# Performance work log

Hardware: AMD Instinct MI355X
Metric: run time of the kernel (lower is better)

## Reference

```python
import jax, jax.numpy as jnp
import numpy as np

NEG_SLOPE = 0.2  # PyG GATConv default negative_slope


def gat_conv(x, src, dst, W, a_src, a_dst, b, n_nodes, concat):
    # x: [N, F_in]; W: [F_in, H*C]; a_src/a_dst: [H, C]; b: [H*C] or [C]
    H, C = a_src.shape
    h = (x @ W).reshape(n_nodes, H, C)                      # [N, H, C]
    al_src = jnp.sum(h * a_src[None], axis=-1)              # [N, H]
    al_dst = jnp.sum(h * a_dst[None], axis=-1)              # [N, H]
    e = jax.nn.leaky_relu(al_src[src] + al_dst[dst], NEG_SLOPE)  # [E, H]
    # segment softmax over incoming edges of each destination node
    m = jax.ops.segment_max(e, dst, num_segments=n_nodes)  # [N, H]
    ex = jnp.exp(e - m[dst])                                # [E, H]
    s = jax.ops.segment_sum(ex, dst, num_segments=n_nodes)  # [N, H]
    alpha = ex / s[dst]                                     # [E, H]
    msg = h[src] * alpha[:, :, None]                        # [E, H, C]
    out = jax.ops.segment_sum(msg, dst, num_segments=n_nodes)  # [N, H, C]
    if concat:
        out = out.reshape(n_nodes, H * C)
    else:
        out = out.mean(axis=1)
    return out + b


def setup_inputs() -> dict:
    key = jax.random.key(0)
    ks = jax.random.split(key, 10)
    N, E = 100000, 800000
    F_in, C1, H, C2 = 128, 32, 8, 16
    x = jax.random.normal(ks[0], (N, F_in), dtype=jnp.float32)
    edge_index = jax.random.randint(ks[1], (2, E), 0, N, dtype=jnp.int64)
    s = 0.05
    return {
        "x": x,
        "edge_index": edge_index,
        "W1": jax.random.normal(ks[2], (F_in, H * C1), dtype=jnp.float32) * s,
        "att_src1": jax.random.normal(ks[3], (H, C1), dtype=jnp.float32) * s,
        "att_dst1": jax.random.normal(ks[4], (H, C1), dtype=jnp.float32) * s,
        "b1": jnp.zeros((H * C1,), dtype=jnp.float32),
        "W2": jax.random.normal(ks[5], (H * C1, H * C2), dtype=jnp.float32) * s,
        "att_src2": jax.random.normal(ks[6], (H, C2), dtype=jnp.float32) * s,
        "att_dst2": jax.random.normal(ks[7], (H, C2), dtype=jnp.float32) * s,
        "b2": jnp.zeros((C2,), dtype=jnp.float32),
    }


def reference(x, edge_index, W1, att_src1, att_dst1, b1, W2, att_src2, att_dst2, b2):
    n = x.shape[0]
    # PyG GATConv default add_self_loops=True (same augmented edge set for both layers)
    loops = jnp.arange(n, dtype=edge_index.dtype)
    src = jnp.concatenate([edge_index[0], loops])
    dst = jnp.concatenate([edge_index[1], loops])
    # dropout_p = 0.0 -> dropout is identity (eval-mode math)
    h = gat_conv(x, src, dst, W1, att_src1, att_dst1, b1, n, concat=True)
    h = jax.nn.elu(h)
    out = gat_conv(h, src, dst, W2, att_src2, att_dst2, b2, n, concat=False)
    return jax.nn.log_softmax(out, axis=-1)
```

## Files before the change

### kernel.cpp

```cpp
#include <hip/hip_runtime.h>
#include <cstdint>
#include <cstddef>


typedef short bf16x8 __attribute__((ext_vector_type(8)));
typedef unsigned short u16x8 __attribute__((ext_vector_type(8)));
typedef float f32x4 __attribute__((ext_vector_type(4)));

__device__ inline unsigned short f2bf(float f) {
  unsigned u = __float_as_uint(f);
  unsigned r = (u + 0x7FFFu + ((u >> 16) & 1u)) >> 16;
  return (unsigned short)r;
}
__device__ inline float bf2f(unsigned short s) {
  return __uint_as_float((unsigned)s << 16);
}

__device__ inline unsigned char fp8enc(float x) {
  unsigned u = __float_as_uint(x);
  unsigned s = u >> 31;
  float ax = fminf(fabsf(x), 448.f);
  unsigned em;
  if (ax >= 0.015625f) {
    unsigned b = __float_as_uint(ax);
    unsigned b2 = b + 0x7FFFFu + ((b >> 20) & 1u);
    em = (b2 >> 20) - 960u;
    if (em > 126u) em = 126u;
  } else {
    em = (unsigned)__float2int_rn(ax * 512.f);
  }
  return (unsigned char)((s << 7) | em);
}
__device__ inline float fp8dec_sw(unsigned b8) {
  unsigned s = b8 >> 7, em = b8 & 0x7Fu;
  float fn = __uint_as_float((s << 31) | ((em + 960u) << 20));
  float fd = (float)em * 0.001953125f;
  fd = s ? -fd : fd;
  return em >= 8u ? fn : fd;
}
__device__ inline void fp8dec4(unsigned w, float* out) {
#if __has_builtin(__builtin_amdgcn_cvt_f32_fp8)
  out[0] = __builtin_amdgcn_cvt_f32_fp8(w, 0);
  out[1] = __builtin_amdgcn_cvt_f32_fp8(w, 1);
  out[2] = __builtin_amdgcn_cvt_f32_fp8(w, 2);
  out[3] = __builtin_amdgcn_cvt_f32_fp8(w, 3);
#else
  out[0] = fp8dec_sw(w & 0xFFu);
  out[1] = fp8dec_sw((w >> 8) & 0xFFu);
  out[2] = fp8dec_sw((w >> 16) & 0xFFu);
  out[3] = fp8dec_sw((w >> 24) & 0xFFu);
#endif
}


__global__ __launch_bounds__(256) void detect_kernel(const int* __restrict__ words,
                                                     int E, int* __restrict__ flag) {
  int t = threadIdx.x;
  int n = E < 1024 ? E : 1024;
  int cnt = 0;
  for (int i = t; i < n; i += 256) cnt += (words[2 * i + 1] != 0) ? 1 : 0;
  for (int m = 1; m < 64; m <<= 1) cnt += __shfl_xor(cnt, m);
  if ((t & 63) == 0 && cnt) atomicAdd(flag, cnt);
}

__global__ __launch_bounds__(256) void scan_a(const int* __restrict__ deg,
                                              int* __restrict__ off,
                                              int* __restrict__ bsum, int N) {
  __shared__ int sh[256];
  int b = blockIdx.x, t = threadIdx.x;
  int base = b * 2048 + t * 8;
  int p[8];
  int run = 0;
#pragma unroll
  for (int j = 0; j < 8; ++j) {
    int v = (base + j < N) ? deg[base + j] : 0;
    run += v;
    p[j] = run;
  }
  sh[t] = run;
  __syncthreads();
  for (int d = 1; d < 256; d <<= 1) {
    int x = (t >= d) ? sh[t - d] : 0;
    __syncthreads();
    if (t >= d) sh[t] += x;
    __syncthreads();
  }
  int excl = sh[t] - run;
#pragma unroll
  for (int j = 0; j < 8; ++j)
    if (base + j < N) off[base + j + 1] = excl + p[j];
  if (t == 255) bsum[b] = sh[255];
}

__global__ __launch_bounds__(256) void scan_c(int* __restrict__ off,
                                              const int* __restrict__ bsum,
                                              int N, int nb) {
  __shared__ int sb[64];
  int t = threadIdx.x;
  if (t < 64) {
    int v = (t < nb) ? bsum[t] : 0;
    for (int d = 1; d < 64; d <<= 1) {
      int u = __shfl_up(v, d);
      if (t >= d) v += u;
    }
    sb[t] = v;
  }
  __syncthreads();
  int i = blockIdx.x * 256 + t;
  if (i == 0) off[0] = 0;
  if (i >= 1 && i <= N) {
    int c = (i - 1) / 2048;
    int excl = (c == 0) ? 0 : sb[c - 1];
    off[i] += excl;
  }
}

__global__ __launch_bounds__(256) void fill_kernel(const int* __restrict__ src,
                                                   const int* __restrict__ dst,
                                                   const int* __restrict__ off,
                                                   int* __restrict__ deg,
                                                   int* __restrict__ csr, int ET) {
  int e = blockIdx.x * 256 + threadIdx.x;
  if (e >= ET) return;
  int d = dst[e];
  int p = atomicSub(&deg[d], 1) - 1;
  csr[off[d] + p] = src[e];
}

__device__ inline void pack_one(const float* __restrict__ W,
                                short* __restrict__ Wp, int NOUT, int idx) {
  int NT = NOUT >> 4;
  int j = idx & 7;
  int lane = (idx >> 3) & 63;
  int st = idx >> 9;
  int s = st / NT, t = st - s * NT;
  int k = s * 32 + (lane >> 4) * 8 + j;
  int n = t * 16 + (lane & 15);
  Wp[idx] = (short)f2bf(W[(size_t)k * NOUT + n]);
}

__global__ __launch_bounds__(256) void pack2_kernel(const float* __restrict__ W1,
                                                    short* __restrict__ W1p,
                                                    const float* __restrict__ W2,
                                                    short* __restrict__ W2p) {
  int b = blockIdx.x, t = threadIdx.x;
  if (b < 128) pack_one(W1, W1p, 256, b * 256 + t);
  else         pack_one(W2, W2p, 128, (b - 128) * 256 + t);
}

template <int K, int NOUT, bool AF32>
__device__ void gemm_body(int bx, const void* __restrict__ Av,
                          const short* __restrict__ Bp,
                          unsigned char* __restrict__ Cq,
                          const float* __restrict__ as,
                          const float* __restrict__ ad,
                          float* __restrict__ alsO,
                          float* __restrict__ aldO, int M) {
  constexpr int KS = K / 32;
  constexpr int NT = NOUT / 16;
  constexpr int RST = NOUT + 8;
  constexpr int QST = NOUT + 16;
  constexpr int C = NOUT / 8;
  __shared__ __align__(16) short lds[64 * RST];
  __shared__ __align__(16) unsigned char ldsq[64 * QST];
  const int tid = threadIdx.x;
  const int wave = tid >> 6, lane = tid & 63;
  const int lo = lane & 15, hi = lane >> 4;
  const int rowA = bx * 64 + wave * 16 + lo;
  const bool inb = rowA < M;

  f32x4 acc[NT];
#pragma unroll
  for (int t = 0; t < NT; ++t) acc[t] = (f32x4){0.f, 0.f, 0.f, 0.f};

#pragma unroll
  for (int s = 0; s < KS; ++s) {
    bf16x8 af;
    if constexpr (AF32) {
      const float* Ap = (const float*)Av;
      float v[8];
      if (inb) {
        const float4 x0 = *(const float4*)&Ap[(size_t)rowA * K + s * 32 + hi * 8];
        const float4 x1 = *(const float4*)&Ap[(size_t)rowA * K + s * 32 + hi * 8 + 4];
        v[0] = x0.x; v[1] = x0.y; v[2] = x0.z; v[3] = x0.w;
        v[4] = x1.x; v[5] = x1.y; v[6] = x1.z; v[7] = x1.w;
      } else {
#pragma unroll
        for (int j = 0; j < 8; ++j) v[j] = 0.f;
      }
#pragma unroll
      for (int j = 0; j < 8; ++j) af[j] = (short)f2bf(v[j]);
    } else {
      const short* Ab = (const short*)Av;
      if (inb) {
        af = *(const bf16x8*)&Ab[(size_t)rowA * K + s * 32 + hi * 8];
      } else {
#pragma unroll
        for (int j = 0; j < 8; ++j) af[j] = 0;
      }
    }
#pragma unroll
    for (int t = 0; t < NT; ++t) {
      bf16x8 bf = *(const bf16x8*)&Bp[((size_t)(s * NT + t) * 64 + lane) * 8];
      acc[t] = __builtin_amdgcn_mfma_f32_16x16x32_bf16(af, bf, acc[t], 0, 0, 0);
    }
  }

#pragma unroll
  for (int t = 0; t < NT; ++t)
#pragma unroll
    for (int r = 0; r < 4; ++r) {
      int row = wave * 16 + hi * 4 + r;
      lds[row * RST + t * 16 + lo] = (short)f2bf(acc[t][r]);
      ldsq[row * QST + t * 16 + lo] = fp8enc(acc[t][r]);
    }
  __syncthreads();

  constexpr int CPR = NOUT / 16;
#pragma unroll
  for (int i = 0; i < (64 * CPR) / 256; ++i) {
    int v = i * 256 + tid;
    int r = v / CPR;
    int c = v % CPR;
    int grow = bx * 64 + r;
    if (grow < M)
      *(float4*)&Cq[(size_t)grow * NOUT + c * 16] =
          *(const float4*)&ldsq[r * QST + c * 16];
  }

  constexpr int SEGS = NOUT / 64;
  if (tid < 64 * SEGS) {
    int r = tid / SEGS, seg = tid % SEGS;
    int grow = bx * 64 + r;
    float ps[8], pd[8];
#pragma unroll
    for (int k = 0; k < 8; ++k) { ps[k] = 0.f; pd[k] = 0.f; }
#pragma unroll
    for (int k = 0; k < 8; ++k) {
      int b = seg + SEGS * k;
      u16x8 u = *(const u16x8*)&lds[r * RST + b * 8];
#pragma unroll
      for (int j = 0; j < 8; ++j) {
        float hv = bf2f(u[j]);
        ps[k] = fmaf(hv, as[k * C + seg * 8 + j], ps[k]);
        pd[k] = fmaf(hv, ad[k * C + seg * 8 + j], pd[k]);
      }
    }
#pragma unroll
    for (int d = 1; d < SEGS; d <<= 1)
#pragma unroll
      for (int k = 0; k < 8; ++k) {
        ps[k] += __shfl_xor(ps[k], d);
        pd[k] += __shfl_xor(pd[k], d);
      }
    if (seg == 0 && grow < M) {
      *(float4*)&alsO[(size_t)grow * 8] = make_float4(ps[0], ps[1], ps[2], ps[3]);
      *(float4*)&alsO[(size_t)grow * 8 + 4] = make_float4(ps[4], ps[5], ps[6], ps[7]);
      *(float4*)&aldO[(size_t)grow * 8] = make_float4(pd[0], pd[1], pd[2], pd[3]);
      *(float4*)&aldO[(size_t)grow * 8 + 4] = make_float4(pd[4], pd[5], pd[6], pd[7]);
    }
  }
}

__global__ __launch_bounds__(256) void mega1_kernel(
    const float* __restrict__ x, const short* __restrict__ W1p,
    unsigned char* __restrict__ h1q, const float* __restrict__ as1,
    const float* __restrict__ ad1, float* __restrict__ als,
    float* __restrict__ ald, int M, int gemmGrid,
    const void* __restrict__ ei, int E, int N, const int* __restrict__ flag,
    int* __restrict__ src, int* __restrict__ dst, int* __restrict__ deg) {
  int bx = blockIdx.x;
  if (bx < gemmGrid) {
    gemm_body<128, 256, true>(bx, x, W1p, h1q, as1, ad1, als, ald, M);
  } else {
    int e = (bx - gemmGrid) * 256 + threadIdx.x;
    int ET = E + N;
    if (e >= ET) return;
    int s, d;
    if (e < E) {
      if (flag[0] == 0) {
        const long long* p = (const long long*)ei;
        s = (int)p[e];
        d = (int)p[(size_t)E + e];
      } else {
        const int* p = (const int*)ei;
        s = p[e];
        d = p[E + e];
      }
    } else {
      s = d = e - E;
    }
    src[e] = s;
    dst[e] = d;
    atomicAdd(&deg[d], 1);
  }
}

template <int K, int NOUT, bool AF32>
__global__ __launch_bounds__(256) void mfma_gemm(const void* __restrict__ Av,
                                                 const short* __restrict__ Bp,
                                                 unsigned char* __restrict__ Cq,
                                                 const float* __restrict__ as,
                                                 const float* __restrict__ ad,
                                                 float* __restrict__ alsO,
                                                 float* __restrict__ aldO, int M) {
  gemm_body<K, NOUT, AF32>(blockIdx.x, Av, Bp, Cq, as, ad, alsO, aldO, M);
}

__global__ __launch_bounds__(256) void agg1_kernel(const unsigned char* __restrict__ hq,
                                                   const float* __restrict__ als,
                                                   const float* __restrict__ ald,
                                                   const int* __restrict__ off,
                                                   const int* __restrict__ csr,
                                                   const float* __restrict__ bias,
                                                   short* __restrict__ outb, int N) {
  int wid = blockIdx.x * 4 + (threadIdx.x >> 6);
  if (wid >= N) return;
  int lane = threadIdx.x & 63;
  int rs = off[wid], re = off[wid + 1];
  int es = lane >> 5;
  int gl = lane & 31;
  int head = gl >> 2;
  float aldv = ald[wid * 8 + head];

  float acc[8];
#pragma unroll
  for (int j = 0; j < 8; ++j) acc[j] = 0.f;
  float ws = 0.f;

  int i = rs + es;
  for (; i + 2 < re; i += 4) {
    int s0 = csr[i], s1 = csr[i + 2];
    float e0 = als[s0 * 8 + head] + aldv;
    float e1 = als[s1 * 8 + head] + aldv;
    uint2 u0 = *(const uint2*)&hq[(size_t)s0 * 256 + gl * 8];
    uint2 u1 = *(const uint2*)&hq[(size_t)s1 * 256 + gl * 8];
    e0 = fmaxf(e0, 0.2f * e0);
    e1 = fmaxf(e1, 0.2f * e1);
    float w0 = __expf(e0), w1 = __expf(e1);
    ws += w0 + w1;
    float d0a[4], d0b[4], d1a[4], d1b[4];
    fp8dec4(u0.x, d0a); fp8dec4(u0.y, d0b);
    fp8dec4(u1.x, d1a); fp8dec4(u1.y, d1b);
#pragma unroll
    for (int j = 0; j < 4; ++j) {
      acc[j] = fmaf(w0, d0a[j], acc[j]);
      acc[j + 4] = fmaf(w0, d0b[j], acc[j + 4]);
      acc[j] = fmaf(w1, d1a[j], acc[j]);
      acc[j + 4] = fmaf(w1, d1b[j], acc[j + 4]);
    }
  }
  if (i < re) {
    int s0 = csr[i];
    float e0 = als[s0 * 8 + head] + aldv;
    uint2 u0 = *(const uint2*)&hq[(size_t)s0 * 256 + gl * 8];
    e0 = fmaxf(e0, 0.2f * e0);
    float w0 = __expf(e0);
    ws += w0;
    float d0a[4], d0b[4];
    fp8dec4(u0.x, d0a); fp8dec4(u0.y, d0b);
#pragma unroll
    for (int j = 0; j < 4; ++j) {
      acc[j] = fmaf(w0, d0a[j], acc[j]);
      acc[j + 4] = fmaf(w0, d0b[j], acc[j + 4]);
    }
  }

  ws += __shfl_xor(ws, 32);
#pragma unroll
  for (int j = 0; j < 8; ++j) acc[j] += __shfl_xor(acc[j], 32);
  float inv = 1.f / ws;

  if (lane < 32) {
    u16x8 o;
#pragma unroll
    for (int j = 0; j < 8; ++j) {
      float v = acc[j] * inv + bias[gl * 8 + j];
      o[j] = f2bf(v > 0.f ? v : expm1f(v));
    }
    *(u16x8*)&outb[(size_t)wid * 256 + gl * 8] = o;
  }
}

__global__ __launch_bounds__(256) void agg2_kernel(const unsigned char* __restrict__ hq,
                                                   const float* __restrict__ als,
                                                   const float* __restrict__ ald,
                                                   const int* __restrict__ off,
                                                   const int* __restrict__ csr,
                                                   const float* __restrict__ bias,
                                                   float* __restrict__ out, int N) {
  int wid = blockIdx.x * 4 + (threadIdx.x >> 6);
  if (wid >= N) return;
  int lane = threadIdx.x & 63;
  int rs = off[wid], re = off[wid + 1];
  int es = lane >> 4;
  int gl = lane & 15;
  int head = gl >> 1;
  float aldv = ald[wid * 8 + head];

  float acc[8];
#pragma unroll
  for (int j = 0; j < 8; ++j) acc[j] = 0.f;
  float ws = 0.f;

  int i = rs + es;
  for (; i + 4 < re; i += 8) {
    int s0 = csr[i], s1 = csr[i + 4];
    float e0 = als[s0 * 8 + head] + aldv;
    float e1 = als[s1 * 8 + head] + aldv;
    uint2 u0 = *(const uint2*)&hq[(size_t)s0 * 128 + gl * 8];
    uint2 u1 = *(const uint2*)&hq[(size_t)s1 * 128 + gl * 8];
    e0 = fmaxf(e0, 0.2f * e0);
    e1 = fmaxf(e1, 0.2f * e1);
    float w0 = __expf(e0), w1 = __expf(e1);
    ws += w0 + w1;
    float d0[8], d1[8];
    fp8dec4(u0.x, d0); fp8dec4(u0.y, d0 + 4);
    fp8dec4(u1.x, d1); fp8dec4(u1.y, d1 + 4);
#pragma unroll
    for (int j = 0; j < 8; ++j)
      acc[j] = fmaf(w1, d1[j], fmaf(w0, d0[j], acc[j]));
  }
  if (i < re) {
    int s0 = csr[i];
    float e0 = als[s0 * 8 + head] + aldv;
    uint2 u0 = *(const uint2*)&hq[(size_t)s0 * 128 + gl * 8];
    e0 = fmaxf(e0, 0.2f * e0);
    float w0 = __expf(e0);
    ws += w0;
    float d0[8];
    fp8dec4(u0.x, d0); fp8dec4(u0.y, d0 + 4);
#pragma unroll
    for (int j = 0; j < 8; ++j) acc[j] = fmaf(w0, d0[j], acc[j]);
  }

#pragma unroll
  for (int d = 16; d < 64; d <<= 1) {
    ws += __shfl_xor(ws, d);
#pragma unroll
    for (int j = 0; j < 8; ++j) acc[j] += __shfl_xor(acc[j], d);
  }
  float inv = 1.f / ws;

#pragma unroll
  for (int j = 0; j < 8; ++j) acc[j] *= inv;
#pragma unroll
  for (int d = 2; d <= 8; d <<= 1)
#pragma unroll
    for (int j = 0; j < 8; ++j) acc[j] += __shfl_xor(acc[j], d);
  int p = gl & 1;
  float v[8];
#pragma unroll
  for (int j = 0; j < 8; ++j) v[j] = acc[j] * 0.125f + bias[p * 8 + j];
  float m = v[0];
#pragma unroll
  for (int j = 1; j < 8; ++j) m = fmaxf(m, v[j]);
  m = fmaxf(m, __shfl_xor(m, 1));
  float se = 0.f;
#pragma unroll
  for (int j = 0; j < 8; ++j) se += __expf(v[j] - m);
  se += __shfl_xor(se, 1);
  float lse = m + logf(se);
  if (lane < 2) {
    *(float4*)&out[(size_t)wid * 16 + p * 8] =
        make_float4(v[0] - lse, v[1] - lse, v[2] - lse, v[3] - lse);
    *(float4*)&out[(size_t)wid * 16 + p * 8 + 4] =
        make_float4(v[4] - lse, v[5] - lse, v[6] - lse, v[7] - lse);
  }
}


extern "C" void kernel_launch(void* const* d_in, const int* in_sizes, int n_in,
                              void* d_out, int out_size, void* d_ws, size_t ws_size,
                              hipStream_t stream) {
  const float* x = (const float*)d_in[0];
  const void* ei = d_in[1];
  const float* W1 = (const float*)d_in[2];
  const float* as1 = (const float*)d_in[3];
  const float* ad1 = (const float*)d_in[4];
  const float* b1 = (const float*)d_in[5];
  const float* W2 = (const float*)d_in[6];
  const float* as2 = (const float*)d_in[7];
  const float* ad2 = (const float*)d_in[8];
  const float* b2 = (const float*)d_in[9];
  float* out = (float*)d_out;

  const int N = out_size / 16;
  const int E = in_sizes[1] / 2;
  const int ET = E + N;

  char* p = (char*)d_ws;
  auto alloc = [&](size_t bytes) {
    char* r = p;
    p += (bytes + 255) & ~(size_t)255;
    return (void*)r;
  };
  unsigned char* h1q = (unsigned char*)alloc((size_t)N * 256);
  short* hactb = (short*)alloc((size_t)N * 256 * 2);
  float* als = (float*)alloc((size_t)N * 8 * 4);
  float* ald = (float*)alloc((size_t)N * 8 * 4);
  int* src32 = (int*)alloc((size_t)ET * 4);
  int* dst32 = (int*)alloc((size_t)ET * 4);
  int* csr = (int*)alloc((size_t)ET * 4);
  int* deg = (int*)alloc((size_t)N * 4);
  int* flag = (int*)alloc(256);
  int* off = (int*)alloc((size_t)(N + 1) * 4);
  int* bsum = (int*)alloc(256 * 4);
  short* W1p = (short*)alloc(128 * 256 * 2);
  short* W2p = (short*)alloc(256 * 128 * 2);
  unsigned char* h2q = h1q;

  hipMemsetAsync(deg, 0, (((size_t)N * 4 + 255) & ~(size_t)255) + 4, stream);

  detect_kernel<<<1, 256, 0, stream>>>((const int*)ei, E, flag);
  pack2_kernel<<<256, 256, 0, stream>>>(W1, W1p, W2, W2p);

  int gemmGrid = (N + 63) / 64;
  int gridET = (ET + 255) / 256;
  int nodeGrid = (N + 3) / 4;
  int nscan = (N + 2047) / 2048;

  mega1_kernel<<<gemmGrid + gridET, 256, 0, stream>>>(
      x, W1p, h1q, as1, ad1, als, ald, N, gemmGrid, ei, E, N, flag, src32,
      dst32, deg);
  scan_a<<<nscan, 256, 0, stream>>>(deg, off, bsum, N);
  scan_c<<<(N + 256) / 256, 256, 0, stream>>>(off, bsum, N, nscan);
  fill_kernel<<<gridET, 256, 0, stream>>>(src32, dst32, off, deg, csr, ET);

  agg1_kernel<<<nodeGrid, 256, 0, stream>>>(h1q, als, ald, off, csr, b1, hactb, N);
  mfma_gemm<256, 128, false><<<gemmGrid, 256, 0, stream>>>(
      hactb, W2p, h2q, as2, ad2, als, ald, N);
  agg2_kernel<<<nodeGrid, 256, 0, stream>>>(h2q, als, ald, off, csr, b2, out, N);
}
```

Before: 324.6 us.

## Split layer-1 aggregation across channel halves and fold detect into pack kernel

```diff
diff --git a/kernel.cpp b/kernel.cpp
--- a/kernel.cpp
+++ b/kernel.cpp
@@ -53,16 +53,6 @@
 }
 
 
-__global__ __launch_bounds__(256) void detect_kernel(const int* __restrict__ words,
-                                                     int E, int* __restrict__ flag) {
-  int t = threadIdx.x;
-  int n = E < 1024 ? E : 1024;
-  int cnt = 0;
-  for (int i = t; i < n; i += 256) cnt += (words[2 * i + 1] != 0) ? 1 : 0;
-  for (int m = 1; m < 64; m <<= 1) cnt += __shfl_xor(cnt, m);
-  if ((t & 63) == 0 && cnt) atomicAdd(flag, cnt);
-}
-
 __global__ __launch_bounds__(256) void scan_a(const int* __restrict__ deg,
                                               int* __restrict__ off,
                                               int* __restrict__ bsum, int N) {
@@ -142,10 +132,21 @@
 __global__ __launch_bounds__(256) void pack2_kernel(const float* __restrict__ W1,
                                                     short* __restrict__ W1p,
                                                     const float* __restrict__ W2,
-                                                    short* __restrict__ W2p) {
+                                                    short* __restrict__ W2p,
+                                                    const int* __restrict__ words,
+                                                    int E, int* __restrict__ flag) {
   int b = blockIdx.x, t = threadIdx.x;
-  if (b < 128) pack_one(W1, W1p, 256, b * 256 + t);
-  else         pack_one(W2, W2p, 128, (b - 128) * 256 + t);
+  if (b < 128) {
+    pack_one(W1, W1p, 256, b * 256 + t);
+  } else if (b < 256) {
+    pack_one(W2, W2p, 128, (b - 128) * 256 + t);
+  } else {
+    int n = E < 1024 ? E : 1024;
+    int cnt = 0;
+    for (int i = t; i < n; i += 256) cnt += (words[2 * i + 1] != 0) ? 1 : 0;
+    for (int m = 1; m < 64; m <<= 1) cnt += __shfl_xor(cnt, m);
+    if ((t & 63) == 0 && cnt) atomicAdd(flag, cnt);
+  }
 }
 
 template <int K, int NOUT, bool AF32>
@@ -316,11 +317,13 @@
                                                    short* __restrict__ outb, int N) {
   int wid = blockIdx.x * 4 + (threadIdx.x >> 6);
   if (wid >= N) return;
+  int cb = blockIdx.y;
   int lane = threadIdx.x & 63;
   int rs = off[wid], re = off[wid + 1];
-  int es = lane >> 5;
-  int gl = lane & 31;
-  int head = gl >> 2;
+  int es = lane >> 4;
+  int gl = lane & 15;
+  int chb = cb * 128 + gl * 8;
+  int head = chb >> 5;
   float aldv = ald[wid * 8 + head];
 
   float acc[8];
@@ -329,56 +332,53 @@
   float ws = 0.f;
 
   int i = rs + es;
-  for (; i + 2 < re; i += 4) {
-    int s0 = csr[i], s1 = csr[i + 2];
-    float e0 = als[s0 * 8 + head] + aldv;
-    float e1 = als[s1 * 8 + head] + aldv;
-    uint2 u0 = *(const uint2*)&hq[(size_t)s0 * 256 + gl * 8];
-    uint2 u1 = *(const uint2*)&hq[(size_t)s1 * 256 + gl * 8];
+  for (; i + 4 < re; i += 8) {
+    int s0 = csr[i], s1 = csr[i + 4];
+    float a0 = als[s0 * 8 + head];
+    float a1 = als[s1 * 8 + head];
+    uint2 u0 = *(const uint2*)&hq[(size_t)s0 * 256 + chb];
+    uint2 u1 = *(const uint2*)&hq[(size_t)s1 * 256 + chb];
+    float e0 = a0 + aldv, e1 = a1 + aldv;
     e0 = fmaxf(e0, 0.2f * e0);
     e1 = fmaxf(e1, 0.2f * e1);
     float w0 = __expf(e0), w1 = __expf(e1);
     ws += w0 + w1;
-    float d0a[4], d0b[4], d1a[4], d1b[4];
-    fp8dec4(u0.x, d0a); fp8dec4(u0.y, d0b);
-    fp8dec4(u1.x, d1a); fp8dec4(u1.y, d1b);
-#pragma unroll
-    for (int j = 0; j < 4; ++j) {
-      acc[j] = fmaf(w0, d0a[j], acc[j]);
-      acc[j + 4] = fmaf(w0, d0b[j], acc[j + 4]);
-      acc[j] = fmaf(w1, d1a[j], acc[j]);
-      acc[j + 4] = fmaf(w1, d1b[j], acc[j + 4]);
-    }
+    float d0[8], d1[8];
+    fp8dec4(u0.x, d0); fp8dec4(u0.y, d0 + 4);
+    fp8dec4(u1.x, d1); fp8dec4(u1.y, d1 + 4);
+#pragma unroll
+    for (int j = 0; j < 8; ++j)
+      acc[j] = fmaf(w1, d1[j], fmaf(w0, d0[j], acc[j]));
   }
   if (i < re) {
     int s0 = csr[i];
     float e0 = als[s0 * 8 + head] + aldv;
-    uint2 u0 = *(const uint2*)&hq[(size_t)s0 * 256 + gl * 8];
+    uint2 u0 = *(const uint2*)&hq[(size_t)s0 * 256 + chb];
     e0 = fmaxf(e0, 0.2f * e0);
     float w0 = __expf(e0);
     ws += w0;
-    float d0a[4], d0b[4];
-    fp8dec4(u0.x, d0a); fp8dec4(u0.y, d0b);
-#pragma unroll
-    for (int j = 0; j < 4; ++j) {
-      acc[j] = fmaf(w0, d0a[j], acc[j]);
-      acc[j + 4] = fmaf(w0, d0b[j], acc[j + 4]);
-    }
-  }
-
-  ws += __shfl_xor(ws, 32);
-#pragma unroll
-  for (int j = 0; j < 8; ++j) acc[j] += __shfl_xor(acc[j], 32);
+    float d0[8];
+    fp8dec4(u0.x, d0); fp8dec4(u0.y, d0 + 4);
+#pragma unroll
+    for (int j = 0; j < 8; ++j) acc[j] = fmaf(w0, d0[j], acc[j]);
+  }
+
+#pragma unroll
+  for (int d = 16; d < 64; d <<= 1) {
+    ws += __shfl_xor(ws, d);
+#pragma unroll
+    for (int j = 0; j < 8; ++j) acc[j] += __shfl_xor(acc[j], d);
+  }
   float inv = 1.f / ws;
 
-  if (lane < 32) {
+  if (lane < 16) {
     u16x8 o;
 #pragma unroll
     for (int j = 0; j < 8; ++j) {
-      float v = acc[j] * inv + bias[gl * 8 + j];
+      float v = acc[j] * inv + bias[chb + j];
       o[j] = f2bf(v > 0.f ? v : expm1f(v));
     }
-    *(u16x8*)&outb[(size_t)wid * 256 + gl * 8] = o;
+    *(u16x8*)&outb[(size_t)wid * 256 + chb] = o;
   }
 }
 
@@ -512,8 +512,7 @@
 
   hipMemsetAsync(deg, 0, (((size_t)N * 4 + 255) & ~(size_t)255) + 4, stream);
 
-  detect_kernel<<<1, 256, 0, stream>>>((const int*)ei, E, flag);
-  pack2_kernel<<<256, 256, 0, stream>>>(W1, W1p, W2, W2p);
+  pack2_kernel<<<257, 256, 0, stream>>>(W1, W1p, W2, W2p, (const int*)ei, E, flag);
 
   int gemmGrid = (N + 63) / 64;
   int gridET = (ET + 255) / 256;
@@ -527,7 +526,8 @@
   scan_c<<<(N + 256) / 256, 256, 0, stream>>>(off, bsum, N, nscan);
   fill_kernel<<<gridET, 256, 0, stream>>>(src32, dst32, off, deg, csr, ET);
 
-  agg1_kernel<<<nodeGrid, 256, 0, stream>>>(h1q, als, ald, off, csr, b1, hactb, N);
+  agg1_kernel<<<dim3(nodeGrid, 2), 256, 0, stream>>>(h1q, als, ald, off, csr,
+                                                     b1, hactb, N);
   mfma_gemm<256, 128, false><<<gemmGrid, 256, 0, stream>>>(
       hactb, W2p, h2q, as2, ad2, als, ald, N);
   agg2_kernel<<<nodeGrid, 256, 0, stream>>>(h2q, als, ald, off, csr, b2, out, N);
```

After: 373.9 us. 1.15x slower.
